# Performance work log

Hardware: AMD Instinct MI355X
Metric: run time of the kernel (lower is better)

Reference implementation:

```python
import jax, jax.numpy as jnp
import numpy as np

EPS = 1e-5


def setup_inputs() -> dict:
    key = jax.random.key(0)
    ks = jax.random.split(key, 12)
    B, C, H, W = 32, 512, 32, 32
    Ci = C // 2
    s_in = 1.0 / np.sqrt(C)
    s_ci = 1.0 / np.sqrt(Ci)
    return {
        "x": jax.random.normal(ks[0], (B, C, H, W), jnp.float32),
        # 1x1 conv weights stored as [out, in]
        "Wg": jax.random.normal(ks[1], (Ci, C), jnp.float32) * s_in,
        "bg": jax.random.normal(ks[2], (Ci,), jnp.float32) * 0.01,
        "Wt": jax.random.normal(ks[3], (Ci, C), jnp.float32) * s_in,
        "bt": jax.random.normal(ks[4], (Ci,), jnp.float32) * 0.01,
        "Wp": jax.random.normal(ks[5], (Ci, C), jnp.float32) * s_in,
        "bp": jax.random.normal(ks[6], (Ci,), jnp.float32) * 0.01,
        "Wz": jax.random.normal(ks[7], (C, Ci), jnp.float32) * s_ci,
        "bz": jax.random.normal(ks[8], (C,), jnp.float32) * 0.01,
        # BN affine params (torch inits these to 0 but we use nonzero for a meaningful baseline)
        "gamma": jax.random.normal(ks[9], (C,), jnp.float32) * 0.1,
        "beta": jax.random.normal(ks[10], (C,), jnp.float32) * 0.1,
    }


def reference(x, Wg, bg, Wt, bt, Wp, bp, Wz, bz, gamma, beta):
    B, C, H, W = x.shape
    N = H * W
    xr = x.reshape(B, C, N)
    # 1x1 conv projections (pure channel GEMMs)
    g_x = jnp.einsum('oc,bcn->bno', Wg, xr) + bg            # [B,N,Ci]
    theta_x = jnp.einsum('oc,bcn->bno', Wt, xr) + bt        # [B,N,Ci]
    phi_x = jnp.einsum('oc,bcn->bon', Wp, xr) + bp[None, :, None]  # [B,Ci,N]
    # full non-local attention over all N=H*W positions
    f = jnp.einsum('bnc,bcm->bnm', theta_x, phi_x)          # [B,N,N]
    attn = jax.nn.softmax(f, axis=-1)
    y = jnp.einsum('bnm,bmo->bon', attn, g_x)               # [B,Ci,N]
    # output 1x1 conv
    w_y = jnp.einsum('oc,bcn->bon', Wz, y) + bz[None, :, None]  # [B,C,N]
    # BatchNorm2d (training mode: batch statistics over B and spatial dims)
    mean = jnp.mean(w_y, axis=(0, 2), keepdims=True)
    var = jnp.var(w_y, axis=(0, 2), keepdims=True)
    w_y = (w_y - mean) / jnp.sqrt(var + EPS)
    w_y = w_y * gamma[None, :, None] + beta[None, :, None]
    return w_y.reshape(B, C, H, W) + x
```

## Files before the change

kernel.cpp:

```cpp
#include <hip/hip_runtime.h>
#include <math.h>

typedef __bf16 bf16;
typedef __bf16 bf16x8 __attribute__((ext_vector_type(8)));
typedef float f32x4 __attribute__((ext_vector_type(4)));
typedef unsigned short u16;
typedef unsigned int u32;

constexpr int BATCH = 32;
constexpr int CH    = 512;
constexpr int CI    = 256;
constexpr int NSP   = 1024;
constexpr int OCH   = 768;
constexpr float EPSV = 1e-5f;

__device__ __forceinline__ void gload_lds16(const bf16* g, bf16* l) {
    __builtin_amdgcn_global_load_lds(
        (const __attribute__((address_space(1))) void*)g,
        (__attribute__((address_space(3))) void*)l, 16, 0, 0);
}

__device__ __forceinline__ u32 pack_bf16(float a, float b) {
    union { bf16 h; u16 u; } ca, cb;
    ca.h = (bf16)a; cb.h = (bf16)b;
    return (u32)ca.u | ((u32)cb.u << 16);
}

__global__ void prep_weights(const float* __restrict__ Wg, const float* __restrict__ Wt,
                             const float* __restrict__ Wp, const float* __restrict__ Wz,
                             bf16* __restrict__ wc, bf16* __restrict__ wz,
                             float* __restrict__ sums) {
    int tid = blockIdx.x * 256 + threadIdx.x;
    if (tid < 1024) sums[tid] = 0.0f;
    if (tid < OCH * CH) {
        int r = tid / CH, c = tid % CH;
        float v;
        if (r < 256)      v = Wt[r * CH + c];
        else if (r < 512) v = Wp[(r - 256) * CH + c];
        else              v = Wg[(r - 512) * CH + c];
        wc[(size_t)(c >> 6) * (OCH * 64) + r * 64 + (c & 63)] = (bf16)v;
    } else {
        int t2 = tid - OCH * CH;
        if (t2 < CH * CI) {
            int r = t2 / CI, o = t2 % CI;
            wz[(size_t)(o >> 6) * (CH * 64) + r * 64 + (o & 63)] = (bf16)Wz[r * CI + o];
        }
    }
}

__global__ void transpose_x(const float* __restrict__ x, bf16* __restrict__ xb) {
    __shared__ bf16 tile[64][64];
    int b = blockIdx.z, kt = blockIdx.y, nb = blockIdx.x;
    int t = threadIdx.x;
    {
        int c_loc = t >> 2;
        int nq = t & 3;
        const float* src = x + ((size_t)b * CH + kt * 64 + c_loc) * NSP + nb * 64 + nq * 16;
        float vv[16];
        *(float4*)(vv + 0)  = *(const float4*)(src + 0);
        *(float4*)(vv + 4)  = *(const float4*)(src + 4);
        *(float4*)(vv + 8)  = *(const float4*)(src + 8);
        *(float4*)(vv + 12) = *(const float4*)(src + 12);
        int nbase = nq * 16;
        #pragma unroll
        for (int i = 0; i < 16; ++i) tile[nbase + i][c_loc] = (bf16)vv[i];
    }
    __syncthreads();
    {
        int n_loc = t >> 2;
        int cq = t & 3;
        bf16* dst = xb + ((((size_t)b * 8 + kt) * NSP) + nb * 64 + n_loc) * 64 + cq * 16;
        *(uint4*)(dst)     = *(const uint4*)&tile[n_loc][cq * 16];
        *(uint4*)(dst + 8) = *(const uint4*)&tile[n_loc][cq * 16 + 8];
    }
}

__launch_bounds__(256, 2)
__global__ void proj_gemm(const bf16* __restrict__ xb, const bf16* __restrict__ wc,
                          const float* __restrict__ bt, const float* __restrict__ bp,
                          const float* __restrict__ bg,
                          bf16* __restrict__ theta, bf16* __restrict__ phi_t,
                          bf16* __restrict__ gt_t) {
    constexpr int LDA = 72;
    __shared__ __align__(16) bf16 sm[2 * 128 * LDA];
    bf16* As = sm;
    bf16* Bs = sm + 128 * LDA;
    int b = blockIdx.z;
    int n0 = blockIdx.y * 128;
    int oc0 = blockIdx.x * 128;
    int t = threadIdx.x, lane = t & 63, wid = t >> 6;
    int wm = wid >> 1, wn = wid & 1;
    int l15 = lane & 15, quad = lane >> 4;

    f32x4 acc[4][4] = {};
    for (int kt = 0; kt < 8; ++kt) {
        __syncthreads();
        const bf16* asrc = xb + ((((size_t)b * 8 + kt) * NSP) + n0) * 64;
        const bf16* bsrc = wc + ((size_t)kt * OCH + oc0) * 64;
        for (int s = t; s < 1024; s += 256) {
            int row = s >> 3, c8 = s & 7;
            *(uint4*)&As[row * LDA + c8 * 8] = *(const uint4*)(asrc + (size_t)s * 8);
            *(uint4*)&Bs[row * LDA + c8 * 8] = *(const uint4*)(bsrc + (size_t)s * 8);
        }
        __syncthreads();
        #pragma unroll
        for (int kc = 0; kc < 2; ++kc) {
            bf16x8 af[4], bfv[4];
            #pragma unroll
            for (int i = 0; i < 4; ++i) {
                af[i]  = *(const bf16x8*)&As[(wm * 64 + i * 16 + l15) * LDA + kc * 32 + quad * 8];
                bfv[i] = *(const bf16x8*)&Bs[(wn * 64 + i * 16 + l15) * LDA + kc * 32 + quad * 8];
            }
            #pragma unroll
            for (int i = 0; i < 4; ++i)
                #pragma unroll
                for (int j = 0; j < 4; ++j)
                    acc[i][j] = __builtin_amdgcn_mfma_f32_16x16x32_bf16(af[i], bfv[j], acc[i][j], 0, 0, 0);
        }
    }
    if (oc0 < 256) {
        #pragma unroll
        for (int j = 0; j < 4; ++j) {
            int och = oc0 + wn * 64 + j * 16 + l15;
            float bv = bt[och];
            #pragma unroll
            for (int i = 0; i < 4; ++i) {
                int nrow = n0 + wm * 64 + i * 16 + quad * 4;
                bf16* p = theta + ((size_t)b * NSP + nrow) * CI + och;
                #pragma unroll
                for (int r = 0; r < 4; ++r)
                    p[(size_t)r * CI] = (bf16)(acc[i][j][r] + bv);
            }
        }
    } else if (oc0 < 512) {
        bf16* dstb = phi_t + (size_t)b * 262144;
        #pragma unroll
        for (int j = 0; j < 4; ++j) {
            int och = (oc0 - 256) + wn * 64 + j * 16 + l15;
            float bv = bp[och];
            int kc = och >> 5, qd = (och >> 3) & 3, e = och & 7;
            #pragma unroll
            for (int i = 0; i < 4; ++i) {
                int nrow = n0 + wm * 64 + i * 16 + quad * 4;
                int kt = nrow >> 5, h = (nrow >> 4) & 1;
                bf16* p = dstb + (size_t)kt * 8192 +
                          (size_t)(((h * 8 + kc) * 64 + qd * 16 + quad * 4) * 8) + e;
                #pragma unroll
                for (int r = 0; r < 4; ++r)
                    p[r * 8] = (bf16)(acc[i][j][r] + bv);
            }
        }
    } else {
        constexpr int LT = 136;
        int obase = oc0 - 512;
        __syncthreads();
        bf16* T = sm;
        #pragma unroll
        for (int j = 0; j < 4; ++j) {
            int och = wn * 64 + j * 16 + l15;
            float bv = bg[obase + och];
            #pragma unroll
            for (int i = 0; i < 4; ++i) {
                int nl = wm * 64 + i * 16 + quad * 4;
                bf16 tmp[4];
                #pragma unroll
                for (int r = 0; r < 4; ++r) tmp[r] = (bf16)(acc[i][j][r] + bv);
                *(uint2*)&T[och * LT + nl] = *(const uint2*)tmp;
            }
        }
        __syncthreads();
        bf16* dstb = gt_t + (size_t)b * 262144;
        for (int s = t; s < 2048; s += 256) {
            int row = s >> 4, part = s & 15;
            int o = obase + row;
            int kglob = n0 + part * 8;
            int kt = kglob >> 5, qd = (kglob >> 3) & 3;
            int qa = (2 * qd) & 3, qb = (2 * qd + 1) & 3;
            int jb = (qd & 2) * 2;
            bf16* base = dstb + (size_t)kt * 8192 + (size_t)((o >> 4) * 512 + (o & 15) * 8);
            *(uint2*)(base + qa * 128 + jb) = *(const uint2*)&T[row * LT + part * 8];
            *(uint2*)(base + qb * 128 + jb) = *(const uint2*)&T[row * LT + part * 8 + 4];
        }
    }
}

__launch_bounds__(256, 2)
__global__ void attn_kernel(const bf16* __restrict__ theta, const bf16* __restrict__ phi_t,
                            const bf16* __restrict__ gt_t, bf16* __restrict__ y) {
    __shared__ __align__(16) char smem[65536];

    int id = blockIdx.x;
    int j = id >> 3;
    int qt = j & 15;
    int b = (id & 7) + 8 * (j >> 4);

    int t = threadIdx.x, lane = t & 63, w = t >> 6;
    int l15 = lane & 15, quad = lane >> 4;

    const bf16* ph_b = phi_t + (size_t)b * 262144 + w * 2048 + lane * 8;
    const bf16* gt_b = gt_t + (size_t)b * 262144 + w * 2048 + lane * 8;

    bf16x8 qf[8];
    {
        const bf16* qrow = theta + ((size_t)b * NSP + qt * 64 + w * 16 + l15) * CI;
        #pragma unroll
        for (int kc = 0; kc < 8; ++kc)
            qf[kc] = *(const bf16x8*)(qrow + kc * 32 + quad * 8);
    }

    {
        bf16* kdst = (bf16*)(smem)         + w * 2048;
        bf16* vdst = (bf16*)(smem + 32768) + w * 2048;
        #pragma unroll
        for (int i = 0; i < 4; ++i) {
            gload_lds16(ph_b + i * 512, kdst + i * 512);
            gload_lds16(gt_b + i * 512, vdst + i * 512);
        }
    }
    __syncthreads();

    f32x4 oacc[16] = {};
    float m = -1e30f;
    float ps = 0.0f;

    for (int kt = 0; kt < 32; ++kt) {
        int cur = kt & 1;
        bf16* Kc = (bf16*)(smem + (cur << 14));
        bf16* Vc = (bf16*)(smem + 32768 + (cur << 14));

        if (kt < 31) {
            const bf16* ksrc = ph_b + (size_t)(kt + 1) * 8192;
            const bf16* vsrc = gt_b + (size_t)(kt + 1) * 8192;
            bf16* kdst = (bf16*)(smem + ((1 - cur) << 14)) + w * 2048;
            bf16* vdst = (bf16*)(smem + 32768 + ((1 - cur) << 14)) + w * 2048;
            #pragma unroll
            for (int i = 0; i < 4; ++i) {
                gload_lds16(ksrc + i * 512, kdst + i * 512);
                gload_lds16(vsrc + i * 512, vdst + i * 512);
            }
        }

        f32x4 s0 = {}, s1 = {};
        __builtin_amdgcn_s_setprio(1);
        #pragma unroll
        for (int kc = 0; kc < 8; ++kc) {
            bf16x8 kf0 = *(const bf16x8*)(Kc + kc * 512 + lane * 8);
            bf16x8 kf1 = *(const bf16x8*)(Kc + 4096 + kc * 512 + lane * 8);
            s0 = __builtin_amdgcn_mfma_f32_16x16x32_bf16(kf0, qf[kc], s0, 0, 0, 0);
            s1 = __builtin_amdgcn_mfma_f32_16x16x32_bf16(kf1, qf[kc], s1, 0, 0, 0);
        }
        __builtin_amdgcn_s_setprio(0);

        float c = fmaxf(fmaxf(fmaxf(s0[0], s0[1]), fmaxf(s0[2], s0[3])),
                        fmaxf(fmaxf(s1[0], s1[1]), fmaxf(s1[2], s1[3])));
        c = fmaxf(c, __shfl_xor(c, 16));
        c = fmaxf(c, __shfl_xor(c, 32));
        int flag = (c > m + 8.0f) ? 1 : 0;
        if (__any(flag)) {
            float mn = fmaxf(m, c);
            float alpha = __expf(m - mn);
            m = mn;
            ps *= alpha;
            float a0 = __shfl(alpha, quad * 4 + 0);
            float a1 = __shfl(alpha, quad * 4 + 1);
            float a2 = __shfl(alpha, quad * 4 + 2);
            float a3 = __shfl(alpha, quad * 4 + 3);
            #pragma unroll
            for (int nt = 0; nt < 16; ++nt) {
                oacc[nt][0] *= a0;
                oacc[nt][1] *= a1;
                oacc[nt][2] *= a2;
                oacc[nt][3] *= a3;
            }
        }
        float p0 = __expf(s0[0] - m), p1 = __expf(s0[1] - m);
        float p2 = __expf(s0[2] - m), p3 = __expf(s0[3] - m);
        float p4 = __expf(s1[0] - m), p5 = __expf(s1[1] - m);
        float p6 = __expf(s1[2] - m), p7 = __expf(s1[3] - m);
        ps += ((p0 + p1) + (p2 + p3)) + ((p4 + p5) + (p6 + p7));

        bf16x8 pf;
        {
            union { u32 u[4]; bf16x8 v; } cvt;
            cvt.u[0] = pack_bf16(p0, p1);
            cvt.u[1] = pack_bf16(p2, p3);
            cvt.u[2] = pack_bf16(p4, p5);
            cvt.u[3] = pack_bf16(p6, p7);
            pf = cvt.v;
        }

        __builtin_amdgcn_s_setprio(1);
        #pragma unroll
        for (int nt = 0; nt < 16; ++nt) {
            bf16x8 vf = *(const bf16x8*)(Vc + nt * 512 + lane * 8);
            oacc[nt] = __builtin_amdgcn_mfma_f32_16x16x32_bf16(pf, vf, oacc[nt], 0, 0, 0);
        }
        __builtin_amdgcn_s_setprio(0);

        __syncthreads();
    }

    ps += __shfl_xor(ps, 16);
    ps += __shfl_xor(ps, 32);
    float inv = 1.0f / ps;
    float inv0 = __shfl(inv, quad * 4 + 0);
    float inv1 = __shfl(inv, quad * 4 + 1);
    float inv2 = __shfl(inv, quad * 4 + 2);
    float inv3 = __shfl(inv, quad * 4 + 3);

    int nrow = qt * 64 + w * 16 + quad * 4;
    #pragma unroll
    for (int nt = 0; nt < 16; ++nt) {
        int o = nt * 16 + l15;
        bf16* dst = y + ((((size_t)b * 4 + (o >> 6)) * NSP) + nrow) * 64 + (o & 63);
        dst[0]           = (bf16)(oacc[nt][0] * inv0);
        dst[(size_t)64]  = (bf16)(oacc[nt][1] * inv1);
        dst[(size_t)128] = (bf16)(oacc[nt][2] * inv2);
        dst[(size_t)192] = (bf16)(oacc[nt][3] * inv3);
    }
}

__launch_bounds__(256, 4)
__global__ void out_gemm(const bf16* __restrict__ y, const bf16* __restrict__ wz,
                         const float* __restrict__ bz, float* __restrict__ wy,
                         float* __restrict__ sums) {
    constexpr int LDA = 72;
    __shared__ __align__(16) bf16 As[128 * LDA];
    __shared__ __align__(16) bf16 Bs[128 * LDA];
    __shared__ float redS[128][2], redS2[128][2];
    int b = blockIdx.z;
    int co0 = blockIdx.y * 128;
    int n0 = blockIdx.x * 128;
    int t = threadIdx.x, lane = t & 63, wid = t >> 6;
    int wm = wid >> 1, wn = wid & 1;
    int l15 = lane & 15, quad = lane >> 4;

    f32x4 acc[4][4] = {};
    for (int kt = 0; kt < 4; ++kt) {
        __syncthreads();
        const bf16* asrc = wz + ((size_t)kt * CH + co0) * 64;
        const bf16* bsrc = y + ((((size_t)b * 4 + kt) * NSP) + n0) * 64;
        for (int s = t; s < 1024; s += 256) {
            int row = s >> 3, c8 = s & 7;
            *(uint4*)&As[row * LDA + c8 * 8] = *(const uint4*)(asrc + (size_t)s * 8);
            *(uint4*)&Bs[row * LDA + c8 * 8] = *(const uint4*)(bsrc + (size_t)s * 8);
        }
        __syncthreads();
        #pragma unroll
        for (int kc = 0; kc < 2; ++kc) {
            bf16x8 af[4], bfv[4];
            #pragma unroll
            for (int i = 0; i < 4; ++i) {
                af[i]  = *(const bf16x8*)&As[(wm * 64 + i * 16 + l15) * LDA + kc * 32 + quad * 8];
                bfv[i] = *(const bf16x8*)&Bs[(wn * 64 + i * 16 + l15) * LDA + kc * 32 + quad * 8];
            }
            #pragma unroll
            for (int i = 0; i < 4; ++i)
                #pragma unroll
                for (int j = 0; j < 4; ++j)
                    acc[i][j] = __builtin_amdgcn_mfma_f32_16x16x32_bf16(af[i], bfv[j], acc[i][j], 0, 0, 0);
        }
    }
    #pragma unroll
    for (int i = 0; i < 4; ++i) {
        int cbase = co0 + wm * 64 + i * 16 + quad * 4;
        #pragma unroll
        for (int r = 0; r < 4; ++r) {
            int c = cbase + r;
            float bv = bz[c];
            float s = 0.f, s2 = 0.f;
            #pragma unroll
            for (int jj = 0; jj < 4; ++jj) {
                int n = n0 + wn * 64 + jj * 16 + l15;
                float v = acc[i][jj][r] + bv;
                wy[((size_t)b * CH + c) * NSP + n] = v;
                s += v; s2 += v * v;
            }
            s  += __shfl_xor(s, 1);  s2 += __shfl_xor(s2, 1);
            s  += __shfl_xor(s, 2);  s2 += __shfl_xor(s2, 2);
            s  += __shfl_xor(s, 4);  s2 += __shfl_xor(s2, 4);
            s  += __shfl_xor(s, 8);  s2 += __shfl_xor(s2, 8);
            if (l15 == 0) {
                int cl = wm * 64 + i * 16 + quad * 4 + r;
                redS[cl][wn]  = s;
                redS2[cl][wn] = s2;
            }
        }
    }
    __syncthreads();
    if (t < 128) {
        atomicAdd(&sums[co0 + t],      redS[t][0] + redS[t][1]);
        atomicAdd(&sums[CH + co0 + t], redS2[t][0] + redS2[t][1]);
    }
}

__global__ void bn_finalize(float* __restrict__ out, const float* __restrict__ x,
                            const float* __restrict__ sums,
                            const float* __restrict__ gamma, const float* __restrict__ beta) {
    size_t idx4 = (size_t)blockIdx.x * 256 + threadIdx.x;
    size_t flat = idx4 * 4;
    int ch = (int)((flat >> 10) & 511);
    float S = sums[ch], S2 = sums[CH + ch];
    const float invcnt = 1.0f / (BATCH * NSP);
    float mean = S * invcnt;
    float var = S2 * invcnt - mean * mean;
    float sc = rsqrtf(var + EPSV) * gamma[ch];
    float bi = beta[ch] - mean * sc;
    float4 wv = *(float4*)(out + flat);
    float4 xv = *(const float4*)(x + flat);
    wv.x = wv.x * sc + bi + xv.x;
    wv.y = wv.y * sc + bi + xv.y;
    wv.z = wv.z * sc + bi + xv.z;
    wv.w = wv.w * sc + bi + xv.w;
    *(float4*)(out + flat) = wv;
}

extern "C" void kernel_launch(void* const* d_in, const int* in_sizes, int n_in,
                              void* d_out, int out_size, void* d_ws, size_t ws_size,
                              hipStream_t stream) {
    const float* x     = (const float*)d_in[0];
    const float* Wg    = (const float*)d_in[1];
    const float* bg    = (const float*)d_in[2];
    const float* Wt    = (const float*)d_in[3];
    const float* bt    = (const float*)d_in[4];
    const float* Wp    = (const float*)d_in[5];
    const float* bp    = (const float*)d_in[6];
    const float* Wz    = (const float*)d_in[7];
    const float* bz    = (const float*)d_in[8];
    const float* gamma = (const float*)d_in[9];
    const float* beta  = (const float*)d_in[10];
    float* out = (float*)d_out;

    char* ws = (char*)d_ws;
    bf16*  y_t   = (bf16*)(ws);
    bf16*  g_t   = (bf16*)(ws + 16777216);
    bf16*  wc    = (bf16*)(ws + 33554432);
    bf16*  wzb   = (bf16*)(ws + 34340864);
    float* sums  = (float*)(ws + 34603008);

    char* ob = (char*)d_out;
    bf16* xb    = (bf16*)(ob);
    bf16* theta = (bf16*)(ob + 33554432);
    bf16* phi_t = (bf16*)(ob + 50331648);

    prep_weights<<<dim3(2048), dim3(256), 0, stream>>>(Wg, Wt, Wp, Wz, wc, wzb, sums);
    transpose_x<<<dim3(16, 8, 32), dim3(256), 0, stream>>>(x, xb);
    proj_gemm<<<dim3(6, 8, 32), dim3(256), 0, stream>>>(xb, wc, bt, bp, bg, theta, phi_t, g_t);
    attn_kernel<<<dim3(512), dim3(256), 0, stream>>>(theta, phi_t, g_t, y_t);
    out_gemm<<<dim3(8, 4, 32), dim3(256), 0, stream>>>(y_t, wzb, bz, out, sums);
    bn_finalize<<<dim3(16384), dim3(256), 0, stream>>>(out, x, sums, gamma, beta);
}
```

Baseline: 289.8 us.

## Split KV across wave halves and double queries per wave in attention

The attention kernel now runs 512-thread blocks covering 128 queries each. Every wave handles two 16-query groups, so each K/V fragment read from LDS feeds two MFMAs. The two halves of the block process separate halves of the key sequence (split-K) with their own double-buffered LDS tiles. At the end they merge their softmax max and sum statistics and partial outputs through LDS. This roughly halves LDS traffic per MFMA and per-query K/V staging, but it doubles the accumulator registers under a (512,2) launch bound, which risks spills. The 133KB of shared memory also limits residency to one block per CU, and the cross-half merge adds extra LDS writes and barriers.

```diff
diff --git a/kernel.cpp b/kernel.cpp
--- a/kernel.cpp
+++ b/kernel.cpp
@@ -184,55 +184,58 @@
     }
 }
 
-__launch_bounds__(256, 2)
+__launch_bounds__(512, 2)
 __global__ void attn_kernel(const bf16* __restrict__ theta, const bf16* __restrict__ phi_t,
                             const bf16* __restrict__ gt_t, bf16* __restrict__ y) {
-    __shared__ __align__(16) char smem[65536];
+    __shared__ __align__(16) char smem[133120];
 
     int id = blockIdx.x;
-    int j = id >> 3;
-    int qt = j & 15;
-    int b = (id & 7) + 8 * (j >> 4);
+    int b = (id & 7) + 8 * (id >> 6);
+    int qt = (id >> 3) & 7;
 
     int t = threadIdx.x, lane = t & 63, w = t >> 6;
     int l15 = lane & 15, quad = lane >> 4;
-
-    const bf16* ph_b = phi_t + (size_t)b * 262144 + w * 2048 + lane * 8;
-    const bf16* gt_b = gt_t + (size_t)b * 262144 + w * 2048 + lane * 8;
-
-    bf16x8 qf[8];
+    int qg = w & 3;
+    int h  = w >> 2;
+    int hbase = h << 16;
+
+    const bf16* ph_w = phi_t + (size_t)b * 262144 + (size_t)h * 16 * 8192 + qg * 2048 + lane * 8;
+    const bf16* gt_w = gt_t + (size_t)b * 262144 + (size_t)h * 16 * 8192 + qg * 2048 + lane * 8;
+
+    bf16x8 qf[2][8];
+    #pragma unroll
+    for (int g = 0; g < 2; ++g) {
+        const bf16* qrow = theta + ((size_t)b * NSP + qt * 128 + qg * 32 + g * 16 + l15) * CI;
+        #pragma unroll
+        for (int kc = 0; kc < 8; ++kc)
+            qf[g][kc] = *(const bf16x8*)(qrow + kc * 32 + quad * 8);
+    }
+
     {
-        const bf16* qrow = theta + ((size_t)b * NSP + qt * 64 + w * 16 + l15) * CI;
-        #pragma unroll
-        for (int kc = 0; kc < 8; ++kc)
-            qf[kc] = *(const bf16x8*)(qrow + kc * 32 + quad * 8);
-    }
-
-    {
-        bf16* kdst = (bf16*)(smem)         + w * 2048;
-        bf16* vdst = (bf16*)(smem + 32768) + w * 2048;
+        bf16* kdst = (bf16*)(smem + hbase)         + qg * 2048;
+        bf16* vdst = (bf16*)(smem + hbase + 32768) + qg * 2048;
         #pragma unroll
         for (int i = 0; i < 4; ++i) {
-            gload_lds16(ph_b + i * 512, kdst + i * 512);
-            gload_lds16(gt_b + i * 512, vdst + i * 512);
+            gload_lds16(ph_w + i * 512, kdst + i * 512);
+            gload_lds16(gt_w + i * 512, vdst + i * 512);
         }
     }
     __syncthreads();
 
-    f32x4 oacc[16] = {};
-    float m = -1e30f;
-    float ps = 0.0f;
-
-    for (int kt = 0; kt < 32; ++kt) {
+    f32x4 oacc[2][16] = {};
+    float m[2]  = {-1e30f, -1e30f};
+    float ps[2] = {0.f, 0.f};
+
+    for (int kt = 0; kt < 16; ++kt) {
         int cur = kt & 1;
-        bf16* Kc = (bf16*)(smem + (cur << 14));
-        bf16* Vc = (bf16*)(smem + 32768 + (cur << 14));
-
-        if (kt < 31) {
-            const bf16* ksrc = ph_b + (size_t)(kt + 1) * 8192;
-            const bf16* vsrc = gt_b + (size_t)(kt + 1) * 8192;
-            bf16* kdst = (bf16*)(smem + ((1 - cur) << 14)) + w * 2048;
-            bf16* vdst = (bf16*)(smem + 32768 + ((1 - cur) << 14)) + w * 2048;
+        bf16* Kc = (bf16*)(smem + hbase + (cur << 14));
+        bf16* Vc = (bf16*)(smem + hbase + 32768 + (cur << 14));
+
+        if (kt < 15) {
+            const bf16* ksrc = ph_w + (size_t)(kt + 1) * 8192;
+            const bf16* vsrc = gt_w + (size_t)(kt + 1) * 8192;
+            bf16* kdst = (bf16*)(smem + hbase + ((1 - cur) << 14)) + qg * 2048;
+            bf16* vdst = (bf16*)(smem + hbase + 32768 + ((1 - cur) << 14)) + qg * 2048;
             #pragma unroll
             for (int i = 0; i < 4; ++i) {
                 gload_lds16(ksrc + i * 512, kdst + i * 512);
@@ -240,83 +243,136 @@
             }
         }
 
-        f32x4 s0 = {}, s1 = {};
+        f32x4 s0[2] = {}, s1[2] = {};
         __builtin_amdgcn_s_setprio(1);
         #pragma unroll
         for (int kc = 0; kc < 8; ++kc) {
             bf16x8 kf0 = *(const bf16x8*)(Kc + kc * 512 + lane * 8);
             bf16x8 kf1 = *(const bf16x8*)(Kc + 4096 + kc * 512 + lane * 8);
-            s0 = __builtin_amdgcn_mfma_f32_16x16x32_bf16(kf0, qf[kc], s0, 0, 0, 0);
-            s1 = __builtin_amdgcn_mfma_f32_16x16x32_bf16(kf1, qf[kc], s1, 0, 0, 0);
+            s0[0] = __builtin_amdgcn_mfma_f32_16x16x32_bf16(kf0, qf[0][kc], s0[0], 0, 0, 0);
+            s0[1] = __builtin_amdgcn_mfma_f32_16x16x32_bf16(kf0, qf[1][kc], s0[1], 0, 0, 0);
+            s1[0] = __builtin_amdgcn_mfma_f32_16x16x32_bf16(kf1, qf[0][kc], s1[0], 0, 0, 0);
+            s1[1] = __builtin_amdgcn_mfma_f32_16x16x32_bf16(kf1, qf[1][kc], s1[1], 0, 0, 0);
         }
         __builtin_amdgcn_s_setprio(0);
 
-        float c = fmaxf(fmaxf(fmaxf(s0[0], s0[1]), fmaxf(s0[2], s0[3])),
-                        fmaxf(fmaxf(s1[0], s1[1]), fmaxf(s1[2], s1[3])));
-        c = fmaxf(c, __shfl_xor(c, 16));
-        c = fmaxf(c, __shfl_xor(c, 32));
-        int flag = (c > m + 8.0f) ? 1 : 0;
+        float cm[2];
+        int flag = 0;
+        #pragma unroll
+        for (int g = 0; g < 2; ++g) {
+            float c = fmaxf(fmaxf(fmaxf(s0[g][0], s0[g][1]), fmaxf(s0[g][2], s0[g][3])),
+                            fmaxf(fmaxf(s1[g][0], s1[g][1]), fmaxf(s1[g][2], s1[g][3])));
+            c = fmaxf(c, __shfl_xor(c, 16));
+            c = fmaxf(c, __shfl_xor(c, 32));
+            cm[g] = c;
+            flag |= (c > m[g] + 8.0f) ? 1 : 0;
+        }
         if (__any(flag)) {
-            float mn = fmaxf(m, c);
-            float alpha = __expf(m - mn);
-            m = mn;
-            ps *= alpha;
-            float a0 = __shfl(alpha, quad * 4 + 0);
-            float a1 = __shfl(alpha, quad * 4 + 1);
-            float a2 = __shfl(alpha, quad * 4 + 2);
-            float a3 = __shfl(alpha, quad * 4 + 3);
-            #pragma unroll
-            for (int nt = 0; nt < 16; ++nt) {
-                oacc[nt][0] *= a0;
-                oacc[nt][1] *= a1;
-                oacc[nt][2] *= a2;
-                oacc[nt][3] *= a3;
-            }
-        }
-        float p0 = __expf(s0[0] - m), p1 = __expf(s0[1] - m);
-        float p2 = __expf(s0[2] - m), p3 = __expf(s0[3] - m);
-        float p4 = __expf(s1[0] - m), p5 = __expf(s1[1] - m);
-        float p6 = __expf(s1[2] - m), p7 = __expf(s1[3] - m);
-        ps += ((p0 + p1) + (p2 + p3)) + ((p4 + p5) + (p6 + p7));
-
-        bf16x8 pf;
-        {
+            #pragma unroll
+            for (int g = 0; g < 2; ++g) {
+                float mn = fmaxf(m[g], cm[g]);
+                float alpha = __expf(m[g] - mn);
+                m[g] = mn;
+                ps[g] *= alpha;
+                float a0 = __shfl(alpha, quad * 4 + 0);
+                float a1 = __shfl(alpha, quad * 4 + 1);
+                float a2 = __shfl(alpha, quad * 4 + 2);
+                float a3 = __shfl(alpha, quad * 4 + 3);
+                #pragma unroll
+                for (int nt = 0; nt < 16; ++nt) {
+                    oacc[g][nt][0] *= a0;
+                    oacc[g][nt][1] *= a1;
+                    oacc[g][nt][2] *= a2;
+                    oacc[g][nt][3] *= a3;
+                }
+            }
+        }
+        bf16x8 pf[2];
+        #pragma unroll
+        for (int g = 0; g < 2; ++g) {
+            float p0 = __expf(s0[g][0] - m[g]), p1 = __expf(s0[g][1] - m[g]);
+            float p2 = __expf(s0[g][2] - m[g]), p3 = __expf(s0[g][3] - m[g]);
+            float p4 = __expf(s1[g][0] - m[g]), p5 = __expf(s1[g][1] - m[g]);
+            float p6 = __expf(s1[g][2] - m[g]), p7 = __expf(s1[g][3] - m[g]);
+            ps[g] += ((p0 + p1) + (p2 + p3)) + ((p4 + p5) + (p6 + p7));
             union { u32 u[4]; bf16x8 v; } cvt;
             cvt.u[0] = pack_bf16(p0, p1);
             cvt.u[1] = pack_bf16(p2, p3);
             cvt.u[2] = pack_bf16(p4, p5);
             cvt.u[3] = pack_bf16(p6, p7);
-            pf = cvt.v;
+            pf[g] = cvt.v;
         }
 
         __builtin_amdgcn_s_setprio(1);
         #pragma unroll
         for (int nt = 0; nt < 16; ++nt) {
             bf16x8 vf = *(const bf16x8*)(Vc + nt * 512 + lane * 8);
-            oacc[nt] = __builtin_amdgcn_mfma_f32_16x16x32_bf16(pf, vf, oacc[nt], 0, 0, 0);
+            oacc[0][nt] = __builtin_amdgcn_mfma_f32_16x16x32_bf16(pf[0], vf, oacc[0][nt], 0, 0, 0);
+            oacc[1][nt] = __builtin_amdgcn_mfma_f32_16x16x32_bf16(pf[1], vf, oacc[1][nt], 0, 0, 0);
         }
         __builtin_amdgcn_s_setprio(0);
 
         __syncthreads();
     }
 
-    ps += __shfl_xor(ps, 16);
-    ps += __shfl_xor(ps, 32);
-    float inv = 1.0f / ps;
-    float inv0 = __shfl(inv, quad * 4 + 0);
-    float inv1 = __shfl(inv, quad * 4 + 1);
-    float inv2 = __shfl(inv, quad * 4 + 2);
-    float inv3 = __shfl(inv, quad * 4 + 3);
-
-    int nrow = qt * 64 + w * 16 + quad * 4;
     #pragma unroll
-    for (int nt = 0; nt < 16; ++nt) {
-        int o = nt * 16 + l15;
-        bf16* dst = y + ((((size_t)b * 4 + (o >> 6)) * NSP) + nrow) * 64 + (o & 63);
-        dst[0]           = (bf16)(oacc[nt][0] * inv0);
-        dst[(size_t)64]  = (bf16)(oacc[nt][1] * inv1);
-        dst[(size_t)128] = (bf16)(oacc[nt][2] * inv2);
-        dst[(size_t)192] = (bf16)(oacc[nt][3] * inv3);
+    for (int g = 0; g < 2; ++g) {
+        ps[g] += __shfl_xor(ps[g], 16);
+        ps[g] += __shfl_xor(ps[g], 32);
+    }
+    float* mps = (float*)(smem + 131072);
+    if (quad == 0) {
+        #pragma unroll
+        for (int g = 0; g < 2; ++g) {
+            float2 v2 = make_float2(m[g], ps[g]);
+            *(float2*)&mps[((w * 2 + g) * 16 + l15) * 2] = v2;
+        }
+    }
+    __syncthreads();
+    int pw = w ^ 4;
+    float ar[2][4], ivr[2][4];
+    #pragma unroll
+    for (int g = 0; g < 2; ++g) {
+        float2 o2 = *(const float2*)&mps[((pw * 2 + g) * 16 + l15) * 2];
+        float mf = fmaxf(m[g], o2.x);
+        float a  = __expf(m[g] - mf);
+        float ao = __expf(o2.x - mf);
+        float pd = ps[g] * a + o2.y * ao;
+        float iv = 1.0f / pd;
+        #pragma unroll
+        for (int r = 0; r < 4; ++r) {
+            ar[g][r]  = __shfl(a, quad * 4 + r);
+            ivr[g][r] = __shfl(iv, quad * 4 + r);
+        }
+    }
+    float* oex = (float*)smem;
+    if (h == 1) {
+        #pragma unroll
+        for (int g = 0; g < 2; ++g)
+            #pragma unroll
+            for (int nt = 0; nt < 16; ++nt)
+                #pragma unroll
+                for (int r = 0; r < 4; ++r)
+                    oex[qg * 8192 + (g * 16 + quad * 4 + r) * 256 + nt * 16 + l15] =
+                        oacc[g][nt][r] * ar[g][r];
+    }
+    __syncthreads();
+    if (h == 0) {
+        #pragma unroll
+        for (int g = 0; g < 2; ++g) {
+            int nrow = qt * 128 + qg * 32 + g * 16 + quad * 4;
+            #pragma unroll
+            for (int nt = 0; nt < 16; ++nt) {
+                int o = nt * 16 + l15;
+                bf16* dst = y + ((((size_t)b * 4 + (o >> 6)) * NSP) + nrow) * 64 + (o & 63);
+                #pragma unroll
+                for (int r = 0; r < 4; ++r) {
+                    float v = oacc[g][nt][r] * ar[g][r] +
+                              oex[qg * 8192 + (g * 16 + quad * 4 + r) * 256 + nt * 16 + l15];
+                    dst[(size_t)r * 64] = (bf16)(v * ivr[g][r]);
+                }
+            }
+        }
     }
 }
 
@@ -446,7 +502,7 @@
     prep_weights<<<dim3(2048), dim3(256), 0, stream>>>(Wg, Wt, Wp, Wz, wc, wzb, sums);
     transpose_x<<<dim3(16, 8, 32), dim3(256), 0, stream>>>(x, xb);
     proj_gemm<<<dim3(6, 8, 32), dim3(256), 0, stream>>>(xb, wc, bt, bp, bg, theta, phi_t, g_t);
-    attn_kernel<<<dim3(512), dim3(256), 0, stream>>>(theta, phi_t, g_t, y_t);
+    attn_kernel<<<dim3(256), dim3(512), 0, stream>>>(theta, phi_t, g_t, y_t);
     out_gemm<<<dim3(8, 4, 32), dim3(256), 0, stream>>>(y_t, wzb, bz, out, sums);
     bn_finalize<<<dim3(16384), dim3(256), 0, stream>>>(out, x, sums, gamma, beta);
 }
```

Result: no change. 285.4 us (-1.5%).

## Software-pipeline QK^T one tile ahead with triple-buffered V and exp2 softmax

Applied to the files above, without the earlier changes.

Restructures the attention loop so the QK^T MFMAs for the next key tile are issued before the softmax and PV of the current tile, using two K buffers and three rotating V buffers in a larger LDS allocation. It also folds log2(e) into theta at projection time so the softmax can use exp2 directly, with the rescale threshold adjusted to match. The aim is to overlap softmax VALU work with MFMA work and remove the multiply inside exp. LDS use grows from 64KB to 80KB per block, which may stop two blocks fitting per CU and cut occupancy.

```diff
diff --git a/kernel.cpp b/kernel.cpp
--- a/kernel.cpp
+++ b/kernel.cpp
@@ -13,6 +13,13 @@
 constexpr int NSP   = 1024;
 constexpr int OCH   = 768;
 constexpr float EPSV = 1e-5f;
+constexpr float LOG2E = 1.4426950408889634f;
+
+#if __has_builtin(__builtin_amdgcn_exp2f)
+#define EXP2F(x) __builtin_amdgcn_exp2f(x)
+#else
+#define EXP2F(x) exp2f(x)
+#endif
 
 __device__ __forceinline__ void gload_lds16(const bf16* g, bf16* l) {
     __builtin_amdgcn_global_load_lds(
@@ -129,7 +136,7 @@
                 bf16* p = theta + ((size_t)b * NSP + nrow) * CI + och;
                 #pragma unroll
                 for (int r = 0; r < 4; ++r)
-                    p[(size_t)r * CI] = (bf16)(acc[i][j][r] + bv);
+                    p[(size_t)r * CI] = (bf16)((acc[i][j][r] + bv) * LOG2E);
             }
         }
     } else if (oc0 < 512) {
@@ -184,10 +191,71 @@
     }
 }
 
+
+#define STAGE(TILE, KDST, VDST) {                                           \
+    const bf16* ksrc_ = ph_b + (size_t)(TILE) * 8192;                       \
+    const bf16* vsrc_ = gt_b + (size_t)(TILE) * 8192;                       \
+    bf16* kd_ = (KDST) + w * 2048;                                          \
+    bf16* vd_ = (VDST) + w * 2048;                                          \
+    _Pragma("unroll")                                                       \
+    for (int i_ = 0; i_ < 4; ++i_) {                                        \
+        gload_lds16(ksrc_ + i_ * 512, kd_ + i_ * 512);                      \
+        gload_lds16(vsrc_ + i_ * 512, vd_ + i_ * 512);                      \
+    } }
+
+#define QKT(S0, S1, KBUF) {                                                 \
+    S0 = (f32x4){}; S1 = (f32x4){};                                         \
+    __builtin_amdgcn_s_setprio(1);                                          \
+    _Pragma("unroll")                                                       \
+    for (int kc_ = 0; kc_ < 8; ++kc_) {                                     \
+        bf16x8 kf0_ = *(const bf16x8*)((KBUF) + kc_ * 512 + lane * 8);      \
+        bf16x8 kf1_ = *(const bf16x8*)((KBUF) + 4096 + kc_ * 512 + lane * 8);\
+        S0 = __builtin_amdgcn_mfma_f32_16x16x32_bf16(kf0_, qf[kc_], S0, 0, 0, 0); \
+        S1 = __builtin_amdgcn_mfma_f32_16x16x32_bf16(kf1_, qf[kc_], S1, 0, 0, 0); \
+    }                                                                       \
+    __builtin_amdgcn_s_setprio(0); }
+
+#define SMPV(S0, S1, VBUF) {                                                \
+    float c_ = fmaxf(fmaxf(fmaxf(S0[0], S0[1]), fmaxf(S0[2], S0[3])),       \
+                     fmaxf(fmaxf(S1[0], S1[1]), fmaxf(S1[2], S1[3])));      \
+    c_ = fmaxf(c_, __shfl_xor(c_, 16));                                     \
+    c_ = fmaxf(c_, __shfl_xor(c_, 32));                                     \
+    int flag_ = (c_ > m + 11.5424f) ? 1 : 0;                                \
+    if (__any(flag_)) {                                                     \
+        float mn_ = fmaxf(m, c_);                                           \
+        float al_ = EXP2F(m - mn_);                                         \
+        m = mn_; ps *= al_;                                                 \
+        float a0_ = __shfl(al_, quad * 4 + 0);                              \
+        float a1_ = __shfl(al_, quad * 4 + 1);                              \
+        float a2_ = __shfl(al_, quad * 4 + 2);                              \
+        float a3_ = __shfl(al_, quad * 4 + 3);                              \
+        _Pragma("unroll")                                                   \
+        for (int nt_ = 0; nt_ < 16; ++nt_) {                                \
+            oacc[nt_][0] *= a0_; oacc[nt_][1] *= a1_;                       \
+            oacc[nt_][2] *= a2_; oacc[nt_][3] *= a3_;                       \
+        } }                                                                 \
+    float p0_ = EXP2F(S0[0] - m), p1_ = EXP2F(S0[1] - m);                   \
+    float p2_ = EXP2F(S0[2] - m), p3_ = EXP2F(S0[3] - m);                   \
+    float p4_ = EXP2F(S1[0] - m), p5_ = EXP2F(S1[1] - m);                   \
+    float p6_ = EXP2F(S1[2] - m), p7_ = EXP2F(S1[3] - m);                   \
+    ps += ((p0_ + p1_) + (p2_ + p3_)) + ((p4_ + p5_) + (p6_ + p7_));        \
+    bf16x8 pf_;                                                             \
+    { union { u32 u[4]; bf16x8 v; } cvt_;                                   \
+      cvt_.u[0] = pack_bf16(p0_, p1_); cvt_.u[1] = pack_bf16(p2_, p3_);     \
+      cvt_.u[2] = pack_bf16(p4_, p5_); cvt_.u[3] = pack_bf16(p6_, p7_);     \
+      pf_ = cvt_.v; }                                                       \
+    __builtin_amdgcn_s_setprio(1);                                          \
+    _Pragma("unroll")                                                       \
+    for (int nt_ = 0; nt_ < 16; ++nt_) {                                    \
+        bf16x8 vf_ = *(const bf16x8*)((VBUF) + nt_ * 512 + lane * 8);       \
+        oacc[nt_] = __builtin_amdgcn_mfma_f32_16x16x32_bf16(pf_, vf_, oacc[nt_], 0, 0, 0); \
+    }                                                                       \
+    __builtin_amdgcn_s_setprio(0); }
+
 __launch_bounds__(256, 2)
 __global__ void attn_kernel(const bf16* __restrict__ theta, const bf16* __restrict__ phi_t,
                             const bf16* __restrict__ gt_t, bf16* __restrict__ y) {
-    __shared__ __align__(16) char smem[65536];
+    __shared__ __align__(16) char smem[81920];
 
     int id = blockIdx.x;
     int j = id >> 3;
@@ -208,96 +276,37 @@
             qf[kc] = *(const bf16x8*)(qrow + kc * 32 + quad * 8);
     }
 
-    {
-        bf16* kdst = (bf16*)(smem)         + w * 2048;
-        bf16* vdst = (bf16*)(smem + 32768) + w * 2048;
-        #pragma unroll
-        for (int i = 0; i < 4; ++i) {
-            gload_lds16(ph_b + i * 512, kdst + i * 512);
-            gload_lds16(gt_b + i * 512, vdst + i * 512);
-        }
-    }
+    bf16* KB0 = (bf16*)smem;
+    bf16* KB1 = (bf16*)(smem + 16384);
+    bf16* Va  = (bf16*)(smem + 32768);
+    bf16* Vb  = (bf16*)(smem + 49152);
+    bf16* Vc  = (bf16*)(smem + 65536);
+
+    STAGE(0, KB0, Va);
+    STAGE(1, KB1, Vb);
     __syncthreads();
 
     f32x4 oacc[16] = {};
     float m = -1e30f;
     float ps = 0.0f;
-
-    for (int kt = 0; kt < 32; ++kt) {
-        int cur = kt & 1;
-        bf16* Kc = (bf16*)(smem + (cur << 14));
-        bf16* Vc = (bf16*)(smem + 32768 + (cur << 14));
-
-        if (kt < 31) {
-            const bf16* ksrc = ph_b + (size_t)(kt + 1) * 8192;
-            const bf16* vsrc = gt_b + (size_t)(kt + 1) * 8192;
-            bf16* kdst = (bf16*)(smem + ((1 - cur) << 14)) + w * 2048;
-            bf16* vdst = (bf16*)(smem + 32768 + ((1 - cur) << 14)) + w * 2048;
-            #pragma unroll
-            for (int i = 0; i < 4; ++i) {
-                gload_lds16(ksrc + i * 512, kdst + i * 512);
-                gload_lds16(vsrc + i * 512, vdst + i * 512);
-            }
-        }
-
-        f32x4 s0 = {}, s1 = {};
-        __builtin_amdgcn_s_setprio(1);
-        #pragma unroll
-        for (int kc = 0; kc < 8; ++kc) {
-            bf16x8 kf0 = *(const bf16x8*)(Kc + kc * 512 + lane * 8);
-            bf16x8 kf1 = *(const bf16x8*)(Kc + 4096 + kc * 512 + lane * 8);
-            s0 = __builtin_amdgcn_mfma_f32_16x16x32_bf16(kf0, qf[kc], s0, 0, 0, 0);
-            s1 = __builtin_amdgcn_mfma_f32_16x16x32_bf16(kf1, qf[kc], s1, 0, 0, 0);
-        }
-        __builtin_amdgcn_s_setprio(0);
-
-        float c = fmaxf(fmaxf(fmaxf(s0[0], s0[1]), fmaxf(s0[2], s0[3])),
-                        fmaxf(fmaxf(s1[0], s1[1]), fmaxf(s1[2], s1[3])));
-        c = fmaxf(c, __shfl_xor(c, 16));
-        c = fmaxf(c, __shfl_xor(c, 32));
-        int flag = (c > m + 8.0f) ? 1 : 0;
-        if (__any(flag)) {
-            float mn = fmaxf(m, c);
-            float alpha = __expf(m - mn);
-            m = mn;
-            ps *= alpha;
-            float a0 = __shfl(alpha, quad * 4 + 0);
-            float a1 = __shfl(alpha, quad * 4 + 1);
-            float a2 = __shfl(alpha, quad * 4 + 2);
-            float a3 = __shfl(alpha, quad * 4 + 3);
-            #pragma unroll
-            for (int nt = 0; nt < 16; ++nt) {
-                oacc[nt][0] *= a0;
-                oacc[nt][1] *= a1;
-                oacc[nt][2] *= a2;
-                oacc[nt][3] *= a3;
-            }
-        }
-        float p0 = __expf(s0[0] - m), p1 = __expf(s0[1] - m);
-        float p2 = __expf(s0[2] - m), p3 = __expf(s0[3] - m);
-        float p4 = __expf(s1[0] - m), p5 = __expf(s1[1] - m);
-        float p6 = __expf(s1[2] - m), p7 = __expf(s1[3] - m);
-        ps += ((p0 + p1) + (p2 + p3)) + ((p4 + p5) + (p6 + p7));
-
-        bf16x8 pf;
-        {
-            union { u32 u[4]; bf16x8 v; } cvt;
-            cvt.u[0] = pack_bf16(p0, p1);
-            cvt.u[1] = pack_bf16(p2, p3);
-            cvt.u[2] = pack_bf16(p4, p5);
-            cvt.u[3] = pack_bf16(p6, p7);
-            pf = cvt.v;
-        }
-
-        __builtin_amdgcn_s_setprio(1);
-        #pragma unroll
-        for (int nt = 0; nt < 16; ++nt) {
-            bf16x8 vf = *(const bf16x8*)(Vc + nt * 512 + lane * 8);
-            oacc[nt] = __builtin_amdgcn_mfma_f32_16x16x32_bf16(pf, vf, oacc[nt], 0, 0, 0);
-        }
-        __builtin_amdgcn_s_setprio(0);
-
-        __syncthreads();
+    f32x4 sA0, sA1, sB0, sB1;
+
+    QKT(sA0, sA1, KB0);
+    __syncthreads();
+
+    for (int kt2 = 0; kt2 < 32; kt2 += 2) {
+        if (kt2 < 30) STAGE(kt2 + 2, KB0, Vc);
+        QKT(sB0, sB1, KB1);
+        SMPV(sA0, sA1, Va);
+        __syncthreads();
+        { bf16* tmp = Va; Va = Vb; Vb = Vc; Vc = tmp; }
+        if (kt2 < 30) {
+            STAGE(kt2 + 3, KB1, Vc);
+            QKT(sA0, sA1, KB0);
+        }
+        SMPV(sB0, sB1, Va);
+        __syncthreads();
+        { bf16* tmp = Va; Va = Vb; Vb = Vc; Vc = tmp; }
     }
 
     ps += __shfl_xor(ps, 16);
```

New measurement: 290.0 us. No clear change (+0.1%).
